# Performance work log

Measured on AMD Instinct MI355X. Metric: run time of the kernel, lower is better.

Reference implementation:

```python
import jax, jax.numpy as jnp
import numpy as np

N_NODES = 50000
N_EDGES = 800000
NUM_LAYERS = 3
NF, EF, QD, H, TD, NT = 256, 64, 128, 64, 32, 64
C = 1.0
EPS = 1e-15


def _expmap0(u, c):
    sc = jnp.sqrt(c)
    n = jnp.maximum(jnp.linalg.norm(u, axis=-1, keepdims=True), EPS)
    return jnp.tanh(sc * n) * u / (sc * n)


def _logmap0(x, c):
    sc = jnp.sqrt(c)
    n = jnp.maximum(jnp.linalg.norm(x, axis=-1, keepdims=True), EPS)
    p = jnp.minimum(sc * n, 1.0 - 1e-5)
    return jnp.arctanh(p) * x / (sc * n)


def setup_inputs() -> dict:
    key = jax.random.key(0)
    ks = jax.random.split(key, 24)
    d = {}
    d['node_features'] = jax.random.normal(ks[0], (N_NODES, NF), jnp.float32)
    d['edge_descriptor'] = jax.random.normal(ks[1], (NT, EF), jnp.float32)
    d['query'] = jax.random.normal(ks[2], (QD,), jnp.float32)
    # params
    d['Wn'] = jax.random.normal(ks[3], (NF, H), jnp.float32) * 0.05  # xavier gain 0.05 in source
    d['bn'] = jnp.zeros((H,), jnp.float32)
    d['tangent_scale'] = jnp.asarray(0.5, jnp.float32)
    d['Wq'] = jax.random.normal(ks[4], (QD, H), jnp.float32) * 0.05
    d['bq'] = jnp.zeros((H,), jnp.float32)
    d['Ws'] = jax.random.normal(ks[5], (EF, TD), jnp.float32) * 0.1
    d['bs'] = jnp.zeros((TD,), jnp.float32)
    d['attn_a'] = jax.random.normal(ks[6], (NUM_LAYERS, 2 * H + TD), jnp.float32) * 0.1
    d['Wmp'] = jax.random.normal(ks[7], (NUM_LAYERS, H, H), jnp.float32) * 0.1
    d['bmp'] = jnp.zeros((NUM_LAYERS, H), jnp.float32)
    d['Wns1'] = jax.random.normal(ks[8], (2 * H, H), jnp.float32) * 0.1
    d['bns1'] = jnp.zeros((H,), jnp.float32)
    d['Wns2'] = jax.random.normal(ks[9], (H, 1), jnp.float32) * 0.1
    d['bns2'] = jnp.zeros((1,), jnp.float32)
    d['Wes1'] = jax.random.normal(ks[10], (2 * H + TD + H, H), jnp.float32) * 0.1
    d['bes1'] = jnp.zeros((H,), jnp.float32)
    d['Wes2'] = jax.random.normal(ks[11], (H, 1), jnp.float32) * 0.1
    d['bes2'] = jnp.zeros((1,), jnp.float32)
    d['edge_index'] = jax.random.randint(ks[12], (2, N_EDGES), 0, N_NODES, jnp.int32)
    d['edge_type'] = jax.random.randint(ks[13], (N_EDGES,), 0, NT, jnp.int32)
    return d


def reference(node_features, edge_descriptor, query, Wn, bn, tangent_scale, Wq, bq,
              Ws, bs, attn_a, Wmp, bmp, Wns1, bns1, Wns2, bns2,
              Wes1, bes1, Wes2, bes2, edge_index, edge_type):
    c = C
    src, dst = edge_index[0], edge_index[1]
    N = node_features.shape[0]
    # node_in + tangent scale + expmap0 onto Poincare ball
    h = _expmap0((node_features @ Wn + bn) * tangent_scale, c)
    q = query @ Wq + bq                       # (H,)
    type_emb = jnp.tanh(edge_descriptor @ Ws + bs)  # (NT, TD) schema encoder
    te = type_emb[edge_type]                  # (E, TD)
    for l in range(NUM_LAYERS):
        ht = _logmap0(h, c)                   # work in tangent space
        feat = jnp.concatenate([ht[src], ht[dst], te], axis=-1)  # (E, 2H+TD)
        s = jax.nn.leaky_relu(feat @ attn_a[l], 0.2)             # (E,)
        m = jax.ops.segment_max(jax.lax.stop_gradient(s), dst, num_segments=N)
        ex = jnp.exp(s - m[dst])
        denom = jax.ops.segment_sum(ex, dst, num_segments=N)
        alpha = ex / (denom[dst] + EPS)       # softmax over incoming edges
        msg = ht @ Wmp[l] + bmp[l]            # (N, H) transform once, gather per-edge
        agg = jax.ops.segment_sum(alpha[:, None] * msg[src], dst, num_segments=N)
        h = _expmap0(jax.nn.relu(agg), c)
    h_flat = _logmap0(h, c)
    q_node = jnp.broadcast_to(q, (N, H))
    node_logits = (jax.nn.relu(jnp.concatenate([h_flat, q_node], -1) @ Wns1 + bns1) @ Wns2 + bns2)[:, 0]
    node_scores = jax.nn.sigmoid(node_logits)
    E = src.shape[0]
    q_edge = jnp.broadcast_to(q, (E, H))
    efeat = jnp.concatenate([h_flat[src], h_flat[dst], te, q_edge], -1)  # (E, 2H+TD+H)
    edge_logits = (jax.nn.relu(efeat @ Wes1 + bes1) @ Wes2 + bes2)[:, 0]
    edge_scores = jax.nn.sigmoid(edge_logits)
    return node_scores, edge_scores, h, type_emb
```

## Files before the change

kernel.cpp:

```cpp
#include <hip/hip_runtime.h>
#include <math.h>

#define NN 50000
#define NE 800000
#define NFD 256
#define HD 64
#define QDD 128
#define TDD 32
#define NTT 64
#define NLAY 3
#define LCLAMP 6.1030340f
#define NBUCK 196
#define SBUCK 6144
#define NPAD (NBUCK * SBUCK)
#define EPB 4096
#define NBINBLK 196
#define PST 72

typedef unsigned int uint;
typedef unsigned short ushort;
typedef __attribute__((ext_vector_type(8))) short bf16x8;
typedef __attribute__((ext_vector_type(4))) float f32x4;

__device__ __forceinline__ ushort f2bf(float f) {
  uint u = __float_as_uint(f);
  uint r = (u + 0x7FFFu + ((u >> 16) & 1u)) >> 16;
  return (ushort)r;
}
__device__ __forceinline__ short f2bfs(float f) { return (short)f2bf(f); }
__device__ __forceinline__ float bf2f(short s) { return __uint_as_float(((uint)(ushort)s) << 16); }
__device__ __forceinline__ float bflo(uint w) { return __uint_as_float(w << 16); }
__device__ __forceinline__ float bfhi(uint w) { return __uint_as_float(w & 0xFFFF0000u); }

__device__ __forceinline__ bf16x8 frag_f32(const float* p) {
  float4 a = *(const float4*)p;
  float4 b = *(const float4*)(p + 4);
  bf16x8 r;
  r[0] = f2bfs(a.x); r[1] = f2bfs(a.y); r[2] = f2bfs(a.z); r[3] = f2bfs(a.w);
  r[4] = f2bfs(b.x); r[5] = f2bfs(b.y); r[6] = f2bfs(b.z); r[7] = f2bfs(b.w);
  return r;
}
__device__ __forceinline__ bf16x8 bfrag_w(const float* W, int k0, int j0, int lane15, int quad) {
  bf16x8 r;
#pragma unroll
  for (int j = 0; j < 8; ++j) r[j] = f2bfs(W[(k0 + quad * 8 + j) * HD + j0 + lane15]);
  return r;
}

__global__ void __launch_bounds__(256) kA(const float* __restrict__ edge_desc, const float* __restrict__ query,
                                          const float* __restrict__ Wq, const float* __restrict__ bq,
                                          const float* __restrict__ Ws, const float* __restrict__ bs,
                                          const float* __restrict__ attn_a,
                                          const float* __restrict__ Wns1, const float* __restrict__ bns1,
                                          const float* __restrict__ Wes1, const float* __restrict__ bes1,
                                          const float* __restrict__ Wmp,
                                          float* __restrict__ out_type_emb,
                                          float* __restrict__ qb, float* __restrict__ ta3,
                                          ushort* __restrict__ Te2bf, ushort* __restrict__ WmpPk) {
  __shared__ float te_l[NTT * TDD];
  __shared__ float q_l[HD];
  __shared__ float qe_l[HD];
  int t = threadIdx.x;
  if (t < HD) {
    float acc = bq[t];
    for (int k = 0; k < QDD; ++k) acc += query[k] * Wq[k * HD + t];
    q_l[t] = acc;
  }
  for (int idx = t; idx < NTT * TDD; idx += 256) {
    int ty = idx / TDD, d = idx % TDD;
    float acc = bs[d];
    for (int k = 0; k < 64; ++k) acc += edge_desc[ty * 64 + k] * Ws[k * TDD + d];
    float v = tanhf(acc);
    te_l[idx] = v;
    out_type_emb[idx] = v;
  }
  __syncthreads();
  if (t < NLAY * NTT) {
    int l = t / NTT, ty = t % NTT;
    float acc = 0.f;
    for (int d = 0; d < TDD; ++d) acc += te_l[ty * TDD + d] * attn_a[l * (2 * HD + TDD) + 2 * HD + d];
    ta3[t] = acc;
  }
  if (t < HD) {
    float a1 = bns1[t], a2 = bes1[t];
    for (int k = 0; k < HD; ++k) {
      a1 += q_l[k] * Wns1[(HD + k) * HD + t];
      a2 += q_l[k] * Wes1[(2 * HD + TDD + k) * HD + t];
    }
    qb[t] = a1;
    qe_l[t] = a2;
  }
  for (int idx = t; idx < NLAY * 4 * 2 * 64 * 8; idx += 256) {
    int j = idx & 7, lane = (idx >> 3) & 63, f = (idx >> 9) & 1, jl = idx >> 10;
    int l = jl >> 2, jt = jl & 3, q = lane >> 4, l15 = lane & 15;
    WmpPk[idx] = f2bf(Wmp[l * HD * HD + (f * 32 + q * 8 + j) * HD + jt * 16 + l15]);
  }
  __syncthreads();
  for (int idx = t; idx < NTT * HD; idx += 256) {
    int ty = idx >> 6, j = idx & 63;
    float acc = qe_l[j];
#pragma unroll
    for (int d = 0; d < TDD; ++d) acc += te_l[ty * TDD + d] * Wes1[(2 * HD + d) * HD + j];
    Te2bf[idx] = f2bf(acc);
  }
}

__device__ void d_bin(int bbid,
                      const int* __restrict__ src,
                      const int* __restrict__ dst,
                      const int* __restrict__ etype,
                      int* __restrict__ bucket_cursor,
                      uint2* __restrict__ ebuf) {
  __shared__ int cntl[NBUCK];
  __shared__ int gbase[NBUCK];
  int t = threadIdx.x;
  for (int i = t; i < NBUCK; i += 256) cntl[i] = 0;
  __syncthreads();
  int e0 = bbid * EPB;
  int dd[16];
  uint pk[16];
  int rk[16];
#pragma unroll
  for (int c = 0; c < 4; ++c) {
    int eb = e0 + c * 1024 + t * 4;
    if (eb < NE) {
      int4 s4 = *(const int4*)&src[eb];
      int4 d4 = *(const int4*)&dst[eb];
      int4 y4 = *(const int4*)&etype[eb];
      int ds[4] = {d4.x, d4.y, d4.z, d4.w};
      int ss[4] = {s4.x, s4.y, s4.z, s4.w};
      int ys[4] = {y4.x, y4.y, y4.z, y4.w};
#pragma unroll
      for (int j = 0; j < 4; ++j) {
        int idx = c * 4 + j;
        int d = ds[j];
        dd[idx] = d;
        pk[idx] = (uint)ss[j] | ((uint)ys[j] << 16) | ((uint)(d & 255) << 22);
        rk[idx] = atomicAdd(&cntl[d >> 8], 1);
      }
    } else {
#pragma unroll
      for (int j = 0; j < 4; ++j) dd[c * 4 + j] = -1;
    }
  }
  __syncthreads();
  if (t < NBUCK && cntl[t] > 0)
    gbase[t] = t * SBUCK + atomicAdd(&bucket_cursor[t], cntl[t]);
  __syncthreads();
#pragma unroll
  for (int i = 0; i < 16; ++i) {
    if (dd[i] >= 0) {
      uint eid = (uint)(e0 + ((i >> 2) << 10) + t * 4 + (i & 3));
      ebuf[gbase[dd[i] >> 8] + rk[i]] = make_uint2(pk[i], eid);
    }
  }
}

__device__ void d_proj(int pbid,
                       const float* __restrict__ X,
                       const float* __restrict__ Wn,
                       const float* __restrict__ bn,
                       const float* __restrict__ ts_p,
                       const ushort* __restrict__ WmpPk,
                       const float* __restrict__ bmp0,
                       const float* __restrict__ attn0,
                       ushort* __restrict__ msgbf,
                       float* __restrict__ p_src,
                       float* __restrict__ p_dst) {
  __shared__ ushort buf[2][64 * PST];
  float* st = (float*)&buf[0][0];
  int t = threadIdx.x;
  int lane = t & 63, wv = t >> 6;
  int lane15 = lane & 15, quad = lane >> 4;
  int n0 = pbid * 64;
  int j0 = wv * 16;
  bf16x8 B[8];
#pragma unroll
  for (int fb = 0; fb < 8; ++fb) B[fb] = bfrag_w(Wn, fb * 32, j0, lane15, quad);

  int srow = t >> 2;
  int scg = (t & 3) * 16;
  int grow = n0 + srow; if (grow >= NN) grow = NN - 1;
  const float* xrow = X + (size_t)grow * NFD + scg;

  f32x4 acc[4];
#pragma unroll
  for (int mt = 0; mt < 4; ++mt) acc[mt] = (f32x4){0.f, 0.f, 0.f, 0.f};

  float4 r0 = *(const float4*)(xrow + 0);
  float4 r1 = *(const float4*)(xrow + 4);
  float4 r2 = *(const float4*)(xrow + 8);
  float4 r3 = *(const float4*)(xrow + 12);

  for (int c = 0; c < 4; ++c) {
    ushort* wp = &buf[c & 1][srow * PST + scg];
    uint4 o0, o1;
    o0.x = (uint)f2bf(r0.x) | ((uint)f2bf(r0.y) << 16);
    o0.y = (uint)f2bf(r0.z) | ((uint)f2bf(r0.w) << 16);
    o0.z = (uint)f2bf(r1.x) | ((uint)f2bf(r1.y) << 16);
    o0.w = (uint)f2bf(r1.z) | ((uint)f2bf(r1.w) << 16);
    o1.x = (uint)f2bf(r2.x) | ((uint)f2bf(r2.y) << 16);
    o1.y = (uint)f2bf(r2.z) | ((uint)f2bf(r2.w) << 16);
    o1.z = (uint)f2bf(r3.x) | ((uint)f2bf(r3.y) << 16);
    o1.w = (uint)f2bf(r3.z) | ((uint)f2bf(r3.w) << 16);
    *(uint4*)wp = o0;
    *(uint4*)(wp + 8) = o1;
    if (c < 3) {
      const float* nx = xrow + (c + 1) * 64;
      r0 = *(const float4*)(nx + 0);
      r1 = *(const float4*)(nx + 4);
      r2 = *(const float4*)(nx + 8);
      r3 = *(const float4*)(nx + 12);
    }
    __syncthreads();
    const ushort* bp = &buf[c & 1][0];
#pragma unroll
    for (int mt = 0; mt < 4; ++mt) {
#pragma unroll
      for (int ks = 0; ks < 2; ++ks) {
        bf16x8 A = *(const bf16x8*)&bp[(mt * 16 + lane15) * PST + ks * 32 + quad * 8];
        acc[mt] = __builtin_amdgcn_mfma_f32_16x16x32_bf16(A, B[c * 2 + ks], acc[mt], 0, 0, 0);
      }
    }
  }
  __syncthreads();
  float ts = ts_p[0];
  float vb = bn[j0 + lane15];
#pragma unroll
  for (int mt = 0; mt < 4; ++mt)
#pragma unroll
    for (int i = 0; i < 4; ++i)
      st[(mt * 16 + quad * 4 + i) * PST + j0 + lane15] = (acc[mt][i] + vb) * ts;
  __syncthreads();
  {
    int r = t >> 2, p = t & 3;
    float* rp = &st[r * PST + p * 16];
    float4 v0 = *(const float4*)(rp + 0);
    float4 v1 = *(const float4*)(rp + 4);
    float4 v2 = *(const float4*)(rp + 8);
    float4 v3 = *(const float4*)(rp + 12);
    float ssq = v0.x*v0.x + v0.y*v0.y + v0.z*v0.z + v0.w*v0.w
              + v1.x*v1.x + v1.y*v1.y + v1.z*v1.z + v1.w*v1.w
              + v2.x*v2.x + v2.y*v2.y + v2.z*v2.z + v2.w*v2.w
              + v3.x*v3.x + v3.y*v3.y + v3.z*v3.z + v3.w*v3.w;
    ssq += __shfl_xor(ssq, 1, 64);
    ssq += __shfl_xor(ssq, 2, 64);
    float nu = fmaxf(sqrtf(ssq), 1e-15f);
    float sc = fminf(nu, LCLAMP) / nu;
    *(float4*)(rp + 0) = make_float4(v0.x*sc, v0.y*sc, v0.z*sc, v0.w*sc);
    *(float4*)(rp + 4) = make_float4(v1.x*sc, v1.y*sc, v1.z*sc, v1.w*sc);
    *(float4*)(rp + 8) = make_float4(v2.x*sc, v2.y*sc, v2.z*sc, v2.w*sc);
    *(float4*)(rp + 12) = make_float4(v3.x*sc, v3.y*sc, v3.z*sc, v3.w*sc);
  }
  __syncthreads();
  {
    bf16x8 Bm0[4], Bm1[4];
    float vbm[4];
#pragma unroll
    for (int jt = 0; jt < 4; ++jt) {
      Bm0[jt] = *(const bf16x8*)&WmpPk[((jt * 2 + 0) * 64 + lane) * 8];
      Bm1[jt] = *(const bf16x8*)&WmpPk[((jt * 2 + 1) * 64 + lane) * 8];
      vbm[jt] = bmp0[jt * 16 + lane15];
    }
    int mrow = wv * 16 + lane15;
    bf16x8 A0 = frag_f32(&st[mrow * PST + quad * 8]);
    bf16x8 A1 = frag_f32(&st[mrow * PST + 32 + quad * 8]);
#pragma unroll
    for (int jt = 0; jt < 4; ++jt) {
      f32x4 z = {0.f, 0.f, 0.f, 0.f};
      z = __builtin_amdgcn_mfma_f32_16x16x32_bf16(A0, Bm0[jt], z, 0, 0, 0);
      z = __builtin_amdgcn_mfma_f32_16x16x32_bf16(A1, Bm1[jt], z, 0, 0, 0);
#pragma unroll
      for (int i = 0; i < 4; ++i) {
        int r = n0 + wv * 16 + quad * 4 + i;
        if (r < NN) msgbf[(size_t)r * HD + jt * 16 + lane15] = f2bf(z[i] + vbm[jt]);
      }
    }
    float4 a1l = *(const float4*)&attn0[quad * 8];
    float4 a1h = *(const float4*)&attn0[quad * 8 + 4];
    float4 a1l2 = *(const float4*)&attn0[32 + quad * 8];
    float4 a1h2 = *(const float4*)&attn0[32 + quad * 8 + 4];
    float4 a2l = *(const float4*)&attn0[64 + quad * 8];
    float4 a2h = *(const float4*)&attn0[64 + quad * 8 + 4];
    float4 a2l2 = *(const float4*)&attn0[96 + quad * 8];
    float4 a2h2 = *(const float4*)&attn0[96 + quad * 8 + 4];
    float p1 = bf2f(A0[0])*a1l.x + bf2f(A0[1])*a1l.y + bf2f(A0[2])*a1l.z + bf2f(A0[3])*a1l.w
             + bf2f(A0[4])*a1h.x + bf2f(A0[5])*a1h.y + bf2f(A0[6])*a1h.z + bf2f(A0[7])*a1h.w
             + bf2f(A1[0])*a1l2.x + bf2f(A1[1])*a1l2.y + bf2f(A1[2])*a1l2.z + bf2f(A1[3])*a1l2.w
             + bf2f(A1[4])*a1h2.x + bf2f(A1[5])*a1h2.y + bf2f(A1[6])*a1h2.z + bf2f(A1[7])*a1h2.w;
    float p2 = bf2f(A0[0])*a2l.x + bf2f(A0[1])*a2l.y + bf2f(A0[2])*a2l.z + bf2f(A0[3])*a2l.w
             + bf2f(A0[4])*a2h.x + bf2f(A0[5])*a2h.y + bf2f(A0[6])*a2h.z + bf2f(A0[7])*a2h.w
             + bf2f(A1[0])*a2l2.x + bf2f(A1[1])*a2l2.y + bf2f(A1[2])*a2l2.z + bf2f(A1[3])*a2l2.w
             + bf2f(A1[4])*a2h2.x + bf2f(A1[5])*a2h2.y + bf2f(A1[6])*a2h2.z + bf2f(A1[7])*a2h2.w;
    p1 += __shfl_xor(p1, 16, 64); p1 += __shfl_xor(p1, 32, 64);
    p2 += __shfl_xor(p2, 16, 64); p2 += __shfl_xor(p2, 32, 64);
    int prow = n0 + mrow;
    if (quad == 0 && prow < NN) { p_src[prow] = p1; p_dst[prow] = p2; }
  }
}

__global__ void __launch_bounds__(256) kE(const int* __restrict__ src, const int* __restrict__ dst,
                                          const int* __restrict__ etype, int* __restrict__ bucket_cursor,
                                          uint2* __restrict__ ebuf,
                                          const float* __restrict__ X, const float* __restrict__ Wn,
                                          const float* __restrict__ bn, const float* __restrict__ ts_p,
                                          const ushort* __restrict__ WmpPk, const float* __restrict__ bmp0,
                                          const float* __restrict__ attn0,
                                          ushort* __restrict__ msgbf,
                                          float* __restrict__ p_src, float* __restrict__ p_dst) {
  if (blockIdx.x < NBINBLK)
    d_bin(blockIdx.x, src, dst, etype, bucket_cursor, ebuf);
  else
    d_proj(blockIdx.x - NBINBLK, X, Wn, bn, ts_p, WmpPk, bmp0, attn0, msgbf, p_src, p_dst);
}

__global__ void __launch_bounds__(256) k_scatter2(const int* __restrict__ bucket_cursor,
                                                  const uint2* __restrict__ ebuf,
                                                  uint* __restrict__ csr,
                                                  uint* __restrict__ csr_eid,
                                                  uint2* __restrict__ rdeg) {
  __shared__ int cnt_l[256];
  __shared__ int curs[256];
  __shared__ int wsum[4], woff[4];
  int b = blockIdx.x;
  int t = threadIdx.x;
  int base = b * SBUCK;
  int cb = bucket_cursor[b];
  cnt_l[t] = 0;
  __syncthreads();
  for (int i = t; i < cb; i += 256)
    atomicAdd(&cnt_l[(ebuf[base + i].x >> 22) & 255], 1);
  __syncthreads();
  int v = cnt_l[t];
  int lane = t & 63, wid = t >> 6;
  int x = v;
#pragma unroll
  for (int off = 1; off < 64; off <<= 1) {
    int y = __shfl_up(x, off, 64);
    if (lane >= off) x += y;
  }
  if (lane == 63) wsum[wid] = x;
  __syncthreads();
  if (t == 0) {
    int a = 0;
    for (int i = 0; i < 4; ++i) { woff[i] = a; a += wsum[i]; }
  }
  __syncthreads();
  int loff = woff[wid] + (x - v);
  int n = (b << 8) + t;
  if (n < NN) rdeg[n] = make_uint2((uint)(base + loff), (uint)v);
  curs[t] = base + loff;
  __syncthreads();
  for (int i = t; i < cb; i += 256) {
    uint2 e = ebuf[base + i];
    int j = (e.x >> 22) & 255;
    int pos = atomicAdd(&curs[j], 1);
    csr[pos] = e.x & 0x3FFFFFu;
    csr_eid[pos] = e.y;
  }
}

template <int FUSE>
__global__ void __launch_bounds__(256) k_agg(const uint2* __restrict__ rdeg,
                                             const uint* __restrict__ csr,
                                             const float* __restrict__ p_src,
                                             const float* __restrict__ p_dst,
                                             const float* __restrict__ ta_l,
                                             const ushort* __restrict__ msgbf,
                                             float* __restrict__ s_buf,
                                             const ushort* __restrict__ WmpPk_next,
                                             const float* __restrict__ bmp_next,
                                             const float* __restrict__ attn_next,
                                             ushort* __restrict__ msg_out,
                                             float* __restrict__ p_src_out,
                                             float* __restrict__ p_dst_out,
                                             float* __restrict__ ht_out) {
  __shared__ float v_lds[16][68];
  __shared__ float exs[4][64];
  __shared__ uint  sis[4][64];
  int t = threadIdx.x;
  int lane = t & 63, wv = t >> 6;
  int nloc = t >> 5;
  int half = (lane >> 5) & 1;
  int l32 = lane & 31;
  int lq = lane & 7;
  int lg32 = (lane >> 3) & 3;
  int n = blockIdx.x * 8 + nloc;
  uint2 rd = rdeg[n];
  int start = (int)rd.x;
  int deg = (int)rd.y;
  int end = start + deg;
  float pd = p_dst[n];
  float acc[8];
#pragma unroll
  for (int u = 0; u < 8; ++u) acc[u] = 0.f;
  float exsum = 0.f;

  if (deg <= 32) {
    bool valid = l32 < deg;
    float s = -3.4e38f;
    int sidx = 0;
    if (valid) {
      uint pk = csr[start + l32];
      sidx = (int)(pk & 0xFFFFu);
      int ty = (int)(pk >> 16);
      float v = p_src[sidx] + pd + ta_l[ty];
      s = (v > 0.f) ? v : 0.2f * v;
    }
    float m = s;
#pragma unroll
    for (int off = 16; off >= 1; off >>= 1) m = fmaxf(m, __shfl_xor(m, off, 64));
    float ex = valid ? __expf(s - m) : 0.f;
    exsum = ex;
    if (valid) { exs[wv][lane] = ex; sis[wv][lane] = (uint)sidx; }
    for (int it = 0; it < deg; it += 4) {
      int el = it + lg32;
      if (el < deg) {
        float exk = exs[wv][half * 32 + el];
        int sk = (int)sis[wv][half * 32 + el];
        uint4 mv = *(const uint4*)&msgbf[(size_t)sk * HD + lq * 8];
        acc[0] += exk * bflo(mv.x); acc[1] += exk * bfhi(mv.x);
        acc[2] += exk * bflo(mv.y); acc[3] += exk * bfhi(mv.y);
        acc[4] += exk * bflo(mv.z); acc[5] += exk * bfhi(mv.z);
        acc[6] += exk * bflo(mv.w); acc[7] += exk * bfhi(mv.w);
      }
    }
  } else {
    float m = -3.4e38f;
    for (int base = start; base < end; base += 32) {
      int i = base + l32;
      float s = -3.4e38f;
      if (i < end) {
        uint pk = csr[i];
        int sidx = (int)(pk & 0xFFFFu);
        int ty = (int)(pk >> 16);
        float v = p_src[sidx] + pd + ta_l[ty];
        s = (v > 0.f) ? v : 0.2f * v;
        s_buf[i] = s;
      }
      m = fmaxf(m, s);
    }
#pragma unroll
    for (int off = 16; off >= 1; off >>= 1) m = fmaxf(m, __shfl_xor(m, off, 64));
    for (int base = start; base < end; base += 32) {
      int i = base + l32;
      if (i < end) {
        float ex = __expf(s_buf[i] - m);
        s_buf[i] = ex;
        exsum += ex;
      }
    }
    for (int it = start; it < end; it += 4) {
      int el = it + lg32;
      if (el < end) {
        float exk = s_buf[el];
        int sk = (int)(csr[el] & 0xFFFFu);
        uint4 mv = *(const uint4*)&msgbf[(size_t)sk * HD + lq * 8];
        acc[0] += exk * bflo(mv.x); acc[1] += exk * bfhi(mv.x);
        acc[2] += exk * bflo(mv.y); acc[3] += exk * bfhi(mv.y);
        acc[4] += exk * bflo(mv.z); acc[5] += exk * bfhi(mv.z);
        acc[6] += exk * bflo(mv.w); acc[7] += exk * bfhi(mv.w);
      }
    }
  }
#pragma unroll
  for (int u = 0; u < 8; ++u) {
    acc[u] += __shfl_xor(acc[u], 8, 64);
    acc[u] += __shfl_xor(acc[u], 16, 64);
  }
#pragma unroll
  for (int off = 16; off >= 1; off >>= 1) exsum += __shfl_xor(exsum, off, 64);
  float inv = 1.f / (exsum + 1e-15f);
  float ss = 0.f;
#pragma unroll
  for (int u = 0; u < 8; ++u) {
    float v = fmaxf(acc[u] * inv, 0.f);
    acc[u] = v;
    ss += v * v;
  }
  ss += __shfl_xor(ss, 1, 64);
  ss += __shfl_xor(ss, 2, 64);
  ss += __shfl_xor(ss, 4, 64);
  float nu = fmaxf(sqrtf(ss), 1e-15f);
  float sc = fminf(nu, LCLAMP) / nu;

  if constexpr (FUSE == 0) {
    if (l32 < 8) {
      *(float4*)&ht_out[(size_t)n * HD + l32 * 8] =
          make_float4(acc[0] * sc, acc[1] * sc, acc[2] * sc, acc[3] * sc);
      *(float4*)&ht_out[(size_t)n * HD + l32 * 8 + 4] =
          make_float4(acc[4] * sc, acc[5] * sc, acc[6] * sc, acc[7] * sc);
    }
  } else {
    float hb[8];
#pragma unroll
    for (int u = 0; u < 8; ++u) hb[u] = bf2f((short)f2bf(acc[u] * sc));
    float4 a1a = *(const float4*)&attn_next[lq * 8];
    float4 a1b = *(const float4*)&attn_next[lq * 8 + 4];
    float4 a2a = *(const float4*)&attn_next[64 + lq * 8];
    float4 a2b = *(const float4*)&attn_next[64 + lq * 8 + 4];
    float p1 = hb[0]*a1a.x + hb[1]*a1a.y + hb[2]*a1a.z + hb[3]*a1a.w
             + hb[4]*a1b.x + hb[5]*a1b.y + hb[6]*a1b.z + hb[7]*a1b.w;
    float p2 = hb[0]*a2a.x + hb[1]*a2a.y + hb[2]*a2a.z + hb[3]*a2a.w
             + hb[4]*a2b.x + hb[5]*a2b.y + hb[6]*a2b.z + hb[7]*a2b.w;
    p1 += __shfl_xor(p1, 1, 64); p1 += __shfl_xor(p1, 2, 64); p1 += __shfl_xor(p1, 4, 64);
    p2 += __shfl_xor(p2, 1, 64); p2 += __shfl_xor(p2, 2, 64); p2 += __shfl_xor(p2, 4, 64);
    if (l32 == 0) { p_src_out[n] = p1; p_dst_out[n] = p2; }
    if (l32 < 8) {
      *(float4*)&v_lds[nloc][l32 * 8] =
          make_float4(acc[0] * sc, acc[1] * sc, acc[2] * sc, acc[3] * sc);
      *(float4*)&v_lds[nloc][l32 * 8 + 4] =
          make_float4(acc[4] * sc, acc[5] * sc, acc[6] * sc, acc[7] * sc);
    }
    __syncthreads();
    int lane15 = lane & 15, quad = lane >> 4;
    bf16x8 A0 = frag_f32(&v_lds[lane15][quad * 8]);
    bf16x8 A1 = frag_f32(&v_lds[lane15][32 + quad * 8]);
    bf16x8 B0 = *(const bf16x8*)&WmpPk_next[(wv * 2 + 0) * 512 + lane * 8];
    bf16x8 B1 = *(const bf16x8*)&WmpPk_next[(wv * 2 + 1) * 512 + lane * 8];
    f32x4 z = {0.f, 0.f, 0.f, 0.f};
    z = __builtin_amdgcn_mfma_f32_16x16x32_bf16(A0, B0, z, 0, 0, 0);
    z = __builtin_amdgcn_mfma_f32_16x16x32_bf16(A1, B1, z, 0, 0, 0);
    float vbm = bmp_next[wv * 16 + lane15];
    if (quad < 2) {
      int nb = blockIdx.x * 8;
#pragma unroll
      for (int i = 0; i < 4; ++i)
        msg_out[(size_t)(nb + quad * 4 + i) * HD + wv * 16 + lane15] = f2bf(z[i] + vbm);
    }
  }
}

__global__ void __launch_bounds__(256) k_score(const float* __restrict__ ht,
                                               const float* __restrict__ Wns1,
                                               const float* __restrict__ qb,
                                               const float* __restrict__ Wns2,
                                               const float* __restrict__ bns2,
                                               const float* __restrict__ Wes1,
                                               float* __restrict__ node_scores,
                                               float* __restrict__ h_out,
                                               ushort* __restrict__ Asrc,
                                               ushort* __restrict__ Adst) {
  int t = threadIdx.x;
  int lane = t & 63, wv = t >> 6;
  int lane15 = lane & 15, quad = lane >> 4;
  int n0 = blockIdx.x * 64;
  int m0 = n0 + wv * 16;
  int row = m0 + lane15;
  int rowc = row < NN ? row : NN - 1;
  bf16x8 A0 = frag_f32(ht + (size_t)rowc * HD + quad * 8);
  bf16x8 A1 = frag_f32(ht + (size_t)rowc * HD + 32 + quad * 8);

  {
    f32x4 acc[4];
#pragma unroll
    for (int jt = 0; jt < 4; ++jt) {
      bf16x8 b0 = bfrag_w(Wns1, 0, jt * 16, lane15, quad);
      bf16x8 b1 = bfrag_w(Wns1, 32, jt * 16, lane15, quad);
      f32x4 z = {0.f, 0.f, 0.f, 0.f};
      z = __builtin_amdgcn_mfma_f32_16x16x32_bf16(A0, b0, z, 0, 0, 0);
      z = __builtin_amdgcn_mfma_f32_16x16x32_bf16(A1, b1, z, 0, 0, 0);
      acc[jt] = z;
    }
    float vqb[4], vw2[4];
#pragma unroll
    for (int jt = 0; jt < 4; ++jt) { vqb[jt] = qb[jt * 16 + lane15]; vw2[jt] = Wns2[jt * 16 + lane15]; }
    float b2 = bns2[0];
#pragma unroll
    for (int i = 0; i < 4; ++i) {
      float si = 0.f;
#pragma unroll
      for (int jt = 0; jt < 4; ++jt) si += fmaxf(acc[jt][i] + vqb[jt], 0.f) * vw2[jt];
      si += __shfl_xor(si, 1, 64);
      si += __shfl_xor(si, 2, 64);
      si += __shfl_xor(si, 4, 64);
      si += __shfl_xor(si, 8, 64);
      int r = m0 + quad * 4 + i;
      if (lane15 == 0 && r < NN) node_scores[r] = 1.f / (1.f + __expf(-(si + b2)));
    }
  }
  {
#pragma unroll
    for (int jt = 0; jt < 4; ++jt) {
      bf16x8 b0 = bfrag_w(Wes1, 0, jt * 16, lane15, quad);
      bf16x8 b1 = bfrag_w(Wes1, 32, jt * 16, lane15, quad);
      f32x4 z = {0.f, 0.f, 0.f, 0.f};
      z = __builtin_amdgcn_mfma_f32_16x16x32_bf16(A0, b0, z, 0, 0, 0);
      z = __builtin_amdgcn_mfma_f32_16x16x32_bf16(A1, b1, z, 0, 0, 0);
#pragma unroll
      for (int i = 0; i < 4; ++i) {
        int r = m0 + quad * 4 + i;
        if (r < NN) Asrc[(size_t)r * HD + jt * 16 + lane15] = f2bf(z[i]);
      }
    }
  }
  {
    const float* W = Wes1 + 64 * HD;
#pragma unroll
    for (int jt = 0; jt < 4; ++jt) {
      bf16x8 b0 = bfrag_w(W, 0, jt * 16, lane15, quad);
      bf16x8 b1 = bfrag_w(W, 32, jt * 16, lane15, quad);
      f32x4 z = {0.f, 0.f, 0.f, 0.f};
      z = __builtin_amdgcn_mfma_f32_16x16x32_bf16(A0, b0, z, 0, 0, 0);
      z = __builtin_amdgcn_mfma_f32_16x16x32_bf16(A1, b1, z, 0, 0, 0);
#pragma unroll
      for (int i = 0; i < 4; ++i) {
        int r = m0 + quad * 4 + i;
        if (r < NN) Adst[(size_t)r * HD + jt * 16 + lane15] = f2bf(z[i]);
      }
    }
  }
  {
    int r = t >> 2, p = t & 3;
    int gr = n0 + r;
    int grc = gr < NN ? gr : NN - 1;
    const float* rp = ht + (size_t)grc * HD + p * 16;
    float4 v0 = *(const float4*)(rp + 0);
    float4 v1 = *(const float4*)(rp + 4);
    float4 v2 = *(const float4*)(rp + 8);
    float4 v3 = *(const float4*)(rp + 12);
    float ssq = v0.x*v0.x + v0.y*v0.y + v0.z*v0.z + v0.w*v0.w
              + v1.x*v1.x + v1.y*v1.y + v1.z*v1.z + v1.w*v1.w
              + v2.x*v2.x + v2.y*v2.y + v2.z*v2.z + v2.w*v2.w
              + v3.x*v3.x + v3.y*v3.y + v3.z*v3.z + v3.w*v3.w;
    ssq += __shfl_xor(ssq, 1, 64);
    ssq += __shfl_xor(ssq, 2, 64);
    float nu = fmaxf(sqrtf(ssq), 1e-15f);
    float hs = tanhf(nu) / nu;
    if (gr < NN) {
      float* op = h_out + (size_t)gr * HD + p * 16;
      *(float4*)(op + 0)  = make_float4(v0.x*hs, v0.y*hs, v0.z*hs, v0.w*hs);
      *(float4*)(op + 4)  = make_float4(v1.x*hs, v1.y*hs, v1.z*hs, v1.w*hs);
      *(float4*)(op + 8)  = make_float4(v2.x*hs, v2.y*hs, v2.z*hs, v2.w*hs);
      *(float4*)(op + 12) = make_float4(v3.x*hs, v3.y*hs, v3.z*hs, v3.w*hs);
    }
  }
}

__global__ void __launch_bounds__(256) k_edge(const uint2* __restrict__ rdeg,
                                              const uint* __restrict__ csr,
                                              const uint* __restrict__ csr_eid,
                                              const ushort* __restrict__ Asrc,
                                              const ushort* __restrict__ Adst,
                                              const ushort* __restrict__ Te2bf,
                                              const float* __restrict__ Wes2,
                                              const float* __restrict__ bes2,
                                              float* __restrict__ edge_scores) {
  int t = threadIdx.x;
  int lane = t & 63;
  int n = (blockIdx.x * 256 + t) >> 6;
  if (n >= NN) return;
  int lq = lane & 7, lg = lane >> 3;
  uint2 rd = rdeg[n];
  int start = (int)rd.x;
  int deg = (int)rd.y;
  if (deg == 0) return;
  int end = start + deg;
  uint4 bv = *(const uint4*)&Adst[(size_t)n * HD + lq * 8];
  const float* wp = &Wes2[lq * 8];
  float4 w0 = *(const float4*)wp;
  float4 w1 = *(const float4*)(wp + 4);
  float b2 = bes2[0];
  for (int it = start; it < end; it += 8) {
    int e = it + lg;
    bool valid = e < end;
    float p = 0.f;
    if (valid) {
      uint pk = csr[e];
      int si = (int)(pk & 0xFFFFu);
      int ty = (int)((pk >> 16) & 0x3Fu);
      uint4 av = *(const uint4*)&Asrc[(size_t)si * HD + lq * 8];
      uint4 tv = *(const uint4*)&Te2bf[ty * HD + lq * 8];
      p += fmaxf(bflo(av.x) + bflo(bv.x) + bflo(tv.x), 0.f) * w0.x;
      p += fmaxf(bfhi(av.x) + bfhi(bv.x) + bfhi(tv.x), 0.f) * w0.y;
      p += fmaxf(bflo(av.y) + bflo(bv.y) + bflo(tv.y), 0.f) * w0.z;
      p += fmaxf(bfhi(av.y) + bfhi(bv.y) + bfhi(tv.y), 0.f) * w0.w;
      p += fmaxf(bflo(av.z) + bflo(bv.z) + bflo(tv.z), 0.f) * w1.x;
      p += fmaxf(bfhi(av.z) + bfhi(bv.z) + bfhi(tv.z), 0.f) * w1.y;
      p += fmaxf(bflo(av.w) + bflo(bv.w) + bflo(tv.w), 0.f) * w1.z;
      p += fmaxf(bfhi(av.w) + bfhi(bv.w) + bfhi(tv.w), 0.f) * w1.w;
    }
    p += __shfl_xor(p, 1, 64);
    p += __shfl_xor(p, 2, 64);
    p += __shfl_xor(p, 4, 64);
    if (valid && lq == 0) edge_scores[csr_eid[e]] = 1.f / (1.f + __expf(-(p + b2)));
  }
}

extern "C" void kernel_launch(void* const* d_in, const int* in_sizes, int n_in,
                              void* d_out, int out_size, void* d_ws, size_t ws_size,
                              hipStream_t stream) {
  const float* node_features = (const float*)d_in[0];
  const float* edge_desc = (const float*)d_in[1];
  const float* query = (const float*)d_in[2];
  const float* Wn = (const float*)d_in[3];
  const float* bn = (const float*)d_in[4];
  const float* ts = (const float*)d_in[5];
  const float* Wq = (const float*)d_in[6];
  const float* bq = (const float*)d_in[7];
  const float* Ws_ = (const float*)d_in[8];
  const float* bs = (const float*)d_in[9];
  const float* attn_a = (const float*)d_in[10];
  const float* Wmp = (const float*)d_in[11];
  const float* bmp = (const float*)d_in[12];
  const float* Wns1 = (const float*)d_in[13];
  const float* bns1 = (const float*)d_in[14];
  const float* Wns2 = (const float*)d_in[15];
  const float* bns2 = (const float*)d_in[16];
  const float* Wes1 = (const float*)d_in[17];
  const float* bes1 = (const float*)d_in[18];
  const float* Wes2 = (const float*)d_in[19];
  const float* bes2 = (const float*)d_in[20];
  const int* edge_index = (const int*)d_in[21];
  const int* etype = (const int*)d_in[22];
  const int* src = edge_index;
  const int* dst = edge_index + NE;

  float* out_ns = (float*)d_out;
  float* out_es = out_ns + NN;
  float* out_h = out_es + NE;
  float* out_te = out_h + (size_t)NN * HD;

  char* w = (char*)d_ws;
  auto alloc = [&](size_t bytes) {
    char* p = w;
    w += (bytes + 1023) & ~(size_t)1023;
    return p;
  };
  float* ht_f = (float*)alloc((size_t)NN * HD * 4);
  ushort* msg0 = (ushort*)alloc((size_t)NN * HD * 2);
  ushort* msg1 = (ushort*)alloc((size_t)NN * HD * 2);
  ushort* Asrc = (ushort*)alloc((size_t)NN * HD * 2);
  ushort* Adst = (ushort*)alloc((size_t)NN * HD * 2);
  float* pA = (float*)alloc(NN * 4);
  float* pdA = (float*)alloc(NN * 4);
  float* pB = (float*)alloc(NN * 4);
  float* pdB = (float*)alloc(NN * 4);
  float* s_buf = (float*)alloc((size_t)NPAD * 4);
  float* qb = (float*)alloc(HD * 4);
  float* ta3 = (float*)alloc(NLAY * NTT * 4);
  ushort* Te2bf = (ushort*)alloc(NTT * HD * 2);
  ushort* WmpPk = (ushort*)alloc(NLAY * 4096 * 2);
  int* bucket_cursor = (int*)alloc(NBUCK * 4);
  uint2* rdeg = (uint2*)alloc((size_t)NN * 8);
  uint* csr = (uint*)alloc((size_t)NPAD * 4);
  uint* csr_eid = (uint*)alloc((size_t)NPAD * 4);
  uint2* ebuf = (uint2*)Asrc;

  hipMemsetAsync(bucket_cursor, 0, NBUCK * 4, stream);
  kA<<<1, 256, 0, stream>>>(edge_desc, query, Wq, bq, Ws_, bs, attn_a,
                            Wns1, bns1, Wes1, bes1, Wmp, out_te, qb, ta3, Te2bf, WmpPk);
  kE<<<NBINBLK + (NN + 63) / 64, 256, 0, stream>>>(src, dst, etype, bucket_cursor, ebuf,
                                                   node_features, Wn, bn, ts, WmpPk,
                                                   bmp, attn_a, msg0, pA, pdA);
  k_scatter2<<<NBUCK, 256, 0, stream>>>(bucket_cursor, ebuf, csr, csr_eid, rdeg);

  const int AGG_GRID = NN / 8;
  k_agg<1><<<AGG_GRID, 256, 0, stream>>>(rdeg, csr, pA, pdA, ta3 + 0 * NTT, msg0, s_buf,
                                         WmpPk + 1 * 4096, bmp + 1 * HD,
                                         attn_a + 1 * (2 * HD + TDD),
                                         msg1, pB, pdB, nullptr);
  k_agg<1><<<AGG_GRID, 256, 0, stream>>>(rdeg, csr, pB, pdB, ta3 + 1 * NTT, msg1, s_buf,
                                         WmpPk + 2 * 4096, bmp + 2 * HD,
                                         attn_a + 2 * (2 * HD + TDD),
                                         msg0, pA, pdA, nullptr);
  k_agg<0><<<AGG_GRID, 256, 0, stream>>>(rdeg, csr, pA, pdA, ta3 + 2 * NTT, msg0, s_buf,
                                         nullptr, nullptr, nullptr,
                                         nullptr, nullptr, nullptr, ht_f);

  k_score<<<(NN + 63) / 64, 256, 0, stream>>>(ht_f, Wns1, qb, Wns2, bns2, Wes1,
                                              out_ns, out_h, Asrc, Adst);
  k_edge<<<(NN + 3) / 4, 256, 0, stream>>>(rdeg, csr, csr_eid, Asrc, Adst, Te2bf,
                                           Wes2, bes2, out_es);
}
```

Baseline: 322.3 us.

## Fold setup kernel into binning kernel and fuse scoring into last aggregation

The single-block setup kernel kA becomes an extra block of the combined binning/projection kernel, and d_proj now packs the layer-0 Wmp weights itself instead of reading them pre-packed. The separate k_score kernel is removed: the final aggregation layer keeps the tangent vectors in LDS and directly computes the expmap output, node scores and the Asrc/Adst edge-MLP projections with MFMA, using weights pre-packed to bf16 in setup. This drops two launches and the fp32 ht round trip through global memory. In exchange it adds a block barrier and extra work to the aggregation kernel, and the MFMA tiles use only half their rows because each block holds 8 nodes.

```diff
diff --git a/kernel.cpp b/kernel.cpp
--- a/kernel.cpp
+++ b/kernel.cpp
@@ -15,6 +15,7 @@
 #define NPAD (NBUCK * SBUCK)
 #define EPB 4096
 #define NBINBLK 196
+#define NPROJ 782
 #define PST 72
 
 typedef unsigned int uint;
@@ -47,16 +48,18 @@
   return r;
 }
 
-__global__ void __launch_bounds__(256) kA(const float* __restrict__ edge_desc, const float* __restrict__ query,
-                                          const float* __restrict__ Wq, const float* __restrict__ bq,
-                                          const float* __restrict__ Ws, const float* __restrict__ bs,
-                                          const float* __restrict__ attn_a,
-                                          const float* __restrict__ Wns1, const float* __restrict__ bns1,
-                                          const float* __restrict__ Wes1, const float* __restrict__ bes1,
-                                          const float* __restrict__ Wmp,
-                                          float* __restrict__ out_type_emb,
-                                          float* __restrict__ qb, float* __restrict__ ta3,
-                                          ushort* __restrict__ Te2bf, ushort* __restrict__ WmpPk) {
+__device__ void d_setup(const float* __restrict__ edge_desc, const float* __restrict__ query,
+                        const float* __restrict__ Wq, const float* __restrict__ bq,
+                        const float* __restrict__ Ws, const float* __restrict__ bs,
+                        const float* __restrict__ attn_a,
+                        const float* __restrict__ Wns1, const float* __restrict__ bns1,
+                        const float* __restrict__ Wes1, const float* __restrict__ bes1,
+                        const float* __restrict__ Wmp,
+                        float* __restrict__ out_type_emb,
+                        float* __restrict__ qb, float* __restrict__ ta3,
+                        ushort* __restrict__ Te2bf, ushort* __restrict__ WmpPk,
+                        ushort* __restrict__ WnsPk, ushort* __restrict__ WesaPk,
+                        ushort* __restrict__ WesbPk) {
   __shared__ float te_l[NTT * TDD];
   __shared__ float q_l[HD];
   __shared__ float qe_l[HD];
@@ -94,6 +97,14 @@
     int j = idx & 7, lane = (idx >> 3) & 63, f = (idx >> 9) & 1, jl = idx >> 10;
     int l = jl >> 2, jt = jl & 3, q = lane >> 4, l15 = lane & 15;
     WmpPk[idx] = f2bf(Wmp[l * HD * HD + (f * 32 + q * 8 + j) * HD + jt * 16 + l15]);
+  }
+  for (int idx = t; idx < 4 * 2 * 64 * 8; idx += 256) {
+    int j = idx & 7, lane = (idx >> 3) & 63, f = (idx >> 9) & 1, jt = (idx >> 10) & 3;
+    int q = lane >> 4, l15 = lane & 15;
+    int row = f * 32 + q * 8 + j, col = jt * 16 + l15;
+    WnsPk[idx]  = f2bf(Wns1[row * HD + col]);
+    WesaPk[idx] = f2bf(Wes1[row * HD + col]);
+    WesbPk[idx] = f2bf(Wes1[(64 + row) * HD + col]);
   }
   __syncthreads();
   for (int idx = t; idx < NTT * HD; idx += 256) {
@@ -161,7 +172,7 @@
                        const float* __restrict__ Wn,
                        const float* __restrict__ bn,
                        const float* __restrict__ ts_p,
-                       const ushort* __restrict__ WmpPk,
+                       const float* __restrict__ Wmp0,
                        const float* __restrict__ bmp0,
                        const float* __restrict__ attn0,
                        ushort* __restrict__ msgbf,
@@ -258,8 +269,8 @@
     float vbm[4];
 #pragma unroll
     for (int jt = 0; jt < 4; ++jt) {
-      Bm0[jt] = *(const bf16x8*)&WmpPk[((jt * 2 + 0) * 64 + lane) * 8];
-      Bm1[jt] = *(const bf16x8*)&WmpPk[((jt * 2 + 1) * 64 + lane) * 8];
+      Bm0[jt] = bfrag_w(Wmp0, 0, jt * 16, lane15, quad);
+      Bm1[jt] = bfrag_w(Wmp0, 32, jt * 16, lane15, quad);
       vbm[jt] = bmp0[jt * 16 + lane15];
     }
     int mrow = wv * 16 + lane15;
@@ -304,14 +315,27 @@
                                           uint2* __restrict__ ebuf,
                                           const float* __restrict__ X, const float* __restrict__ Wn,
                                           const float* __restrict__ bn, const float* __restrict__ ts_p,
-                                          const ushort* __restrict__ WmpPk, const float* __restrict__ bmp0,
-                                          const float* __restrict__ attn0,
+                                          const float* __restrict__ Wmp, const float* __restrict__ bmp,
+                                          const float* __restrict__ attn_a,
                                           ushort* __restrict__ msgbf,
-                                          float* __restrict__ p_src, float* __restrict__ p_dst) {
+                                          float* __restrict__ p_src, float* __restrict__ p_dst,
+                                          const float* __restrict__ edge_desc, const float* __restrict__ query,
+                                          const float* __restrict__ Wq, const float* __restrict__ bq,
+                                          const float* __restrict__ Ws, const float* __restrict__ bs,
+                                          const float* __restrict__ Wns1, const float* __restrict__ bns1,
+                                          const float* __restrict__ Wes1, const float* __restrict__ bes1,
+                                          float* __restrict__ out_type_emb,
+                                          float* __restrict__ qb, float* __restrict__ ta3,
+                                          ushort* __restrict__ Te2bf, ushort* __restrict__ WmpPk,
+                                          ushort* __restrict__ WnsPk, ushort* __restrict__ WesaPk,
+                                          ushort* __restrict__ WesbPk) {
   if (blockIdx.x < NBINBLK)
     d_bin(blockIdx.x, src, dst, etype, bucket_cursor, ebuf);
+  else if (blockIdx.x < NBINBLK + NPROJ)
+    d_proj(blockIdx.x - NBINBLK, X, Wn, bn, ts_p, Wmp, bmp, attn_a, msgbf, p_src, p_dst);
   else
-    d_proj(blockIdx.x - NBINBLK, X, Wn, bn, ts_p, WmpPk, bmp0, attn0, msgbf, p_src, p_dst);
+    d_setup(edge_desc, query, Wq, bq, Ws, bs, attn_a, Wns1, bns1, Wes1, bes1, Wmp,
+            out_type_emb, qb, ta3, Te2bf, WmpPk, WnsPk, WesaPk, WesbPk);
 }
 
 __global__ void __launch_bounds__(256) k_scatter2(const int* __restrict__ bucket_cursor,
@@ -374,10 +398,20 @@
                                              ushort* __restrict__ msg_out,
                                              float* __restrict__ p_src_out,
                                              float* __restrict__ p_dst_out,
-                                             float* __restrict__ ht_out) {
+                                             const float* __restrict__ qb,
+                                             const float* __restrict__ Wns2,
+                                             const float* __restrict__ bns2,
+                                             const ushort* __restrict__ WnsPk,
+                                             const ushort* __restrict__ WesaPk,
+                                             const ushort* __restrict__ WesbPk,
+                                             float* __restrict__ node_scores,
+                                             float* __restrict__ h_out,
+                                             ushort* __restrict__ Asrc,
+                                             ushort* __restrict__ Adst) {
   __shared__ float v_lds[16][68];
   __shared__ float exs[4][64];
   __shared__ uint  sis[4][64];
+  __shared__ float sc_part[8][4];
   int t = threadIdx.x;
   int lane = t & 63, wv = t >> 6;
   int nloc = t >> 5;
@@ -486,10 +520,85 @@
 
   if constexpr (FUSE == 0) {
     if (l32 < 8) {
-      *(float4*)&ht_out[(size_t)n * HD + l32 * 8] =
+      *(float4*)&v_lds[nloc][l32 * 8] =
           make_float4(acc[0] * sc, acc[1] * sc, acc[2] * sc, acc[3] * sc);
-      *(float4*)&ht_out[(size_t)n * HD + l32 * 8 + 4] =
+      *(float4*)&v_lds[nloc][l32 * 8 + 4] =
           make_float4(acc[4] * sc, acc[5] * sc, acc[6] * sc, acc[7] * sc);
+    }
+    __syncthreads();
+    int lane15 = lane & 15, quad = lane >> 4;
+    int nb = blockIdx.x * 8;
+    if (t < 32) {
+      int r = t >> 2, p = t & 3;
+      const float* rp = &v_lds[r][p * 16];
+      float4 v0 = *(const float4*)(rp + 0);
+      float4 v1 = *(const float4*)(rp + 4);
+      float4 v2 = *(const float4*)(rp + 8);
+      float4 v3 = *(const float4*)(rp + 12);
+      float ssq = v0.x*v0.x + v0.y*v0.y + v0.z*v0.z + v0.w*v0.w
+                + v1.x*v1.x + v1.y*v1.y + v1.z*v1.z + v1.w*v1.w
+                + v2.x*v2.x + v2.y*v2.y + v2.z*v2.z + v2.w*v2.w
+                + v3.x*v3.x + v3.y*v3.y + v3.z*v3.z + v3.w*v3.w;
+      ssq += __shfl_xor(ssq, 1, 64);
+      ssq += __shfl_xor(ssq, 2, 64);
+      float nu2 = fmaxf(sqrtf(ssq), 1e-15f);
+      float hs = tanhf(nu2) / nu2;
+      float* op = h_out + (size_t)(nb + r) * HD + p * 16;
+      *(float4*)(op + 0)  = make_float4(v0.x*hs, v0.y*hs, v0.z*hs, v0.w*hs);
+      *(float4*)(op + 4)  = make_float4(v1.x*hs, v1.y*hs, v1.z*hs, v1.w*hs);
+      *(float4*)(op + 8)  = make_float4(v2.x*hs, v2.y*hs, v2.z*hs, v2.w*hs);
+      *(float4*)(op + 12) = make_float4(v3.x*hs, v3.y*hs, v3.z*hs, v3.w*hs);
+    }
+    bf16x8 A0 = frag_f32(&v_lds[lane15][quad * 8]);
+    bf16x8 A1 = frag_f32(&v_lds[lane15][32 + quad * 8]);
+    {
+      bf16x8 B0 = *(const bf16x8*)&WnsPk[(wv * 2 + 0) * 512 + lane * 8];
+      bf16x8 B1 = *(const bf16x8*)&WnsPk[(wv * 2 + 1) * 512 + lane * 8];
+      f32x4 z = {0.f, 0.f, 0.f, 0.f};
+      z = __builtin_amdgcn_mfma_f32_16x16x32_bf16(A0, B0, z, 0, 0, 0);
+      z = __builtin_amdgcn_mfma_f32_16x16x32_bf16(A1, B1, z, 0, 0, 0);
+      float vqb = qb[wv * 16 + lane15];
+      float vw2 = Wns2[wv * 16 + lane15];
+      if (quad < 2) {
+#pragma unroll
+        for (int i = 0; i < 4; ++i) {
+          float part = fmaxf(z[i] + vqb, 0.f) * vw2;
+          part += __shfl_xor(part, 1, 64);
+          part += __shfl_xor(part, 2, 64);
+          part += __shfl_xor(part, 4, 64);
+          part += __shfl_xor(part, 8, 64);
+          if (lane15 == 0) sc_part[quad * 4 + i][wv] = part;
+        }
+      }
+    }
+    {
+      bf16x8 B0 = *(const bf16x8*)&WesaPk[(wv * 2 + 0) * 512 + lane * 8];
+      bf16x8 B1 = *(const bf16x8*)&WesaPk[(wv * 2 + 1) * 512 + lane * 8];
+      f32x4 z = {0.f, 0.f, 0.f, 0.f};
+      z = __builtin_amdgcn_mfma_f32_16x16x32_bf16(A0, B0, z, 0, 0, 0);
+      z = __builtin_amdgcn_mfma_f32_16x16x32_bf16(A1, B1, z, 0, 0, 0);
+      if (quad < 2) {
+#pragma unroll
+        for (int i = 0; i < 4; ++i)
+          Asrc[(size_t)(nb + quad * 4 + i) * HD + wv * 16 + lane15] = f2bf(z[i]);
+      }
+    }
+    {
+      bf16x8 B0 = *(const bf16x8*)&WesbPk[(wv * 2 + 0) * 512 + lane * 8];
+      bf16x8 B1 = *(const bf16x8*)&WesbPk[(wv * 2 + 1) * 512 + lane * 8];
+      f32x4 z = {0.f, 0.f, 0.f, 0.f};
+      z = __builtin_amdgcn_mfma_f32_16x16x32_bf16(A0, B0, z, 0, 0, 0);
+      z = __builtin_amdgcn_mfma_f32_16x16x32_bf16(A1, B1, z, 0, 0, 0);
+      if (quad < 2) {
+#pragma unroll
+        for (int i = 0; i < 4; ++i)
+          Adst[(size_t)(nb + quad * 4 + i) * HD + wv * 16 + lane15] = f2bf(z[i]);
+      }
+    }
+    __syncthreads();
+    if (t < 8) {
+      float si = sc_part[t][0] + sc_part[t][1] + sc_part[t][2] + sc_part[t][3];
+      node_scores[nb + t] = 1.f / (1.f + __expf(-(si + bns2[0])));
     }
   } else {
     float hb[8];
@@ -527,112 +636,6 @@
 #pragma unroll
       for (int i = 0; i < 4; ++i)
         msg_out[(size_t)(nb + quad * 4 + i) * HD + wv * 16 + lane15] = f2bf(z[i] + vbm);
-    }
-  }
-}
-
-__global__ void __launch_bounds__(256) k_score(const float* __restrict__ ht,
-                                               const float* __restrict__ Wns1,
-                                               const float* __restrict__ qb,
-                                               const float* __restrict__ Wns2,
-                                               const float* __restrict__ bns2,
-                                               const float* __restrict__ Wes1,
-                                               float* __restrict__ node_scores,
-                                               float* __restrict__ h_out,
-                                               ushort* __restrict__ Asrc,
-                                               ushort* __restrict__ Adst) {
-  int t = threadIdx.x;
-  int lane = t & 63, wv = t >> 6;
-  int lane15 = lane & 15, quad = lane >> 4;
-  int n0 = blockIdx.x * 64;
-  int m0 = n0 + wv * 16;
-  int row = m0 + lane15;
-  int rowc = row < NN ? row : NN - 1;
-  bf16x8 A0 = frag_f32(ht + (size_t)rowc * HD + quad * 8);
-  bf16x8 A1 = frag_f32(ht + (size_t)rowc * HD + 32 + quad * 8);
-
-  {
-    f32x4 acc[4];
-#pragma unroll
-    for (int jt = 0; jt < 4; ++jt) {
-      bf16x8 b0 = bfrag_w(Wns1, 0, jt * 16, lane15, quad);
-      bf16x8 b1 = bfrag_w(Wns1, 32, jt * 16, lane15, quad);
-      f32x4 z = {0.f, 0.f, 0.f, 0.f};
-      z = __builtin_amdgcn_mfma_f32_16x16x32_bf16(A0, b0, z, 0, 0, 0);
-      z = __builtin_amdgcn_mfma_f32_16x16x32_bf16(A1, b1, z, 0, 0, 0);
-      acc[jt] = z;
-    }
-    float vqb[4], vw2[4];
-#pragma unroll
-    for (int jt = 0; jt < 4; ++jt) { vqb[jt] = qb[jt * 16 + lane15]; vw2[jt] = Wns2[jt * 16 + lane15]; }
-    float b2 = bns2[0];
-#pragma unroll
-    for (int i = 0; i < 4; ++i) {
-      float si = 0.f;
-#pragma unroll
-      for (int jt = 0; jt < 4; ++jt) si += fmaxf(acc[jt][i] + vqb[jt], 0.f) * vw2[jt];
-      si += __shfl_xor(si, 1, 64);
-      si += __shfl_xor(si, 2, 64);
-      si += __shfl_xor(si, 4, 64);
-      si += __shfl_xor(si, 8, 64);
-      int r = m0 + quad * 4 + i;
-      if (lane15 == 0 && r < NN) node_scores[r] = 1.f / (1.f + __expf(-(si + b2)));
-    }
-  }
-  {
-#pragma unroll
-    for (int jt = 0; jt < 4; ++jt) {
-      bf16x8 b0 = bfrag_w(Wes1, 0, jt * 16, lane15, quad);
-      bf16x8 b1 = bfrag_w(Wes1, 32, jt * 16, lane15, quad);
-      f32x4 z = {0.f, 0.f, 0.f, 0.f};
-      z = __builtin_amdgcn_mfma_f32_16x16x32_bf16(A0, b0, z, 0, 0, 0);
-      z = __builtin_amdgcn_mfma_f32_16x16x32_bf16(A1, b1, z, 0, 0, 0);
-#pragma unroll
-      for (int i = 0; i < 4; ++i) {
-        int r = m0 + quad * 4 + i;
-        if (r < NN) Asrc[(size_t)r * HD + jt * 16 + lane15] = f2bf(z[i]);
-      }
-    }
-  }
-  {
-    const float* W = Wes1 + 64 * HD;
-#pragma unroll
-    for (int jt = 0; jt < 4; ++jt) {
-      bf16x8 b0 = bfrag_w(W, 0, jt * 16, lane15, quad);
-      bf16x8 b1 = bfrag_w(W, 32, jt * 16, lane15, quad);
-      f32x4 z = {0.f, 0.f, 0.f, 0.f};
-      z = __builtin_amdgcn_mfma_f32_16x16x32_bf16(A0, b0, z, 0, 0, 0);
-      z = __builtin_amdgcn_mfma_f32_16x16x32_bf16(A1, b1, z, 0, 0, 0);
-#pragma unroll
-      for (int i = 0; i < 4; ++i) {
-        int r = m0 + quad * 4 + i;
-        if (r < NN) Adst[(size_t)r * HD + jt * 16 + lane15] = f2bf(z[i]);
-      }
-    }
-  }
-  {
-    int r = t >> 2, p = t & 3;
-    int gr = n0 + r;
-    int grc = gr < NN ? gr : NN - 1;
-    const float* rp = ht + (size_t)grc * HD + p * 16;
-    float4 v0 = *(const float4*)(rp + 0);
-    float4 v1 = *(const float4*)(rp + 4);
-    float4 v2 = *(const float4*)(rp + 8);
-    float4 v3 = *(const float4*)(rp + 12);
-    float ssq = v0.x*v0.x + v0.y*v0.y + v0.z*v0.z + v0.w*v0.w
-              + v1.x*v1.x + v1.y*v1.y + v1.z*v1.z + v1.w*v1.w
-              + v2.x*v2.x + v2.y*v2.y + v2.z*v2.z + v2.w*v2.w
-              + v3.x*v3.x + v3.y*v3.y + v3.z*v3.z + v3.w*v3.w;
-    ssq += __shfl_xor(ssq, 1, 64);
-    ssq += __shfl_xor(ssq, 2, 64);
-    float nu = fmaxf(sqrtf(ssq), 1e-15f);
-    float hs = tanhf(nu) / nu;
-    if (gr < NN) {
-      float* op = h_out + (size_t)gr * HD + p * 16;
-      *(float4*)(op + 0)  = make_float4(v0.x*hs, v0.y*hs, v0.z*hs, v0.w*hs);
-      *(float4*)(op + 4)  = make_float4(v1.x*hs, v1.y*hs, v1.z*hs, v1.w*hs);
-      *(float4*)(op + 8)  = make_float4(v2.x*hs, v2.y*hs, v2.z*hs, v2.w*hs);
-      *(float4*)(op + 12) = make_float4(v3.x*hs, v3.y*hs, v3.z*hs, v3.w*hs);
     }
   }
 }
@@ -727,7 +730,6 @@
     w += (bytes + 1023) & ~(size_t)1023;
     return p;
   };
-  float* ht_f = (float*)alloc((size_t)NN * HD * 4);
   ushort* msg0 = (ushort*)alloc((size_t)NN * HD * 2);
   ushort* msg1 = (ushort*)alloc((size_t)NN * HD * 2);
   ushort* Asrc = (ushort*)alloc((size_t)NN * HD * 2);
@@ -741,6 +743,9 @@
   float* ta3 = (float*)alloc(NLAY * NTT * 4);
   ushort* Te2bf = (ushort*)alloc(NTT * HD * 2);
   ushort* WmpPk = (ushort*)alloc(NLAY * 4096 * 2);
+  ushort* WnsPk = (ushort*)alloc(4096 * 2);
+  ushort* WesaPk = (ushort*)alloc(4096 * 2);
+  ushort* WesbPk = (ushort*)alloc(4096 * 2);
   int* bucket_cursor = (int*)alloc(NBUCK * 4);
   uint2* rdeg = (uint2*)alloc((size_t)NN * 8);
   uint* csr = (uint*)alloc((size_t)NPAD * 4);
@@ -748,28 +753,34 @@
   uint2* ebuf = (uint2*)Asrc;
 
   hipMemsetAsync(bucket_cursor, 0, NBUCK * 4, stream);
-  kA<<<1, 256, 0, stream>>>(edge_desc, query, Wq, bq, Ws_, bs, attn_a,
-                            Wns1, bns1, Wes1, bes1, Wmp, out_te, qb, ta3, Te2bf, WmpPk);
-  kE<<<NBINBLK + (NN + 63) / 64, 256, 0, stream>>>(src, dst, etype, bucket_cursor, ebuf,
-                                                   node_features, Wn, bn, ts, WmpPk,
-                                                   bmp, attn_a, msg0, pA, pdA);
+  kE<<<NBINBLK + NPROJ + 1, 256, 0, stream>>>(src, dst, etype, bucket_cursor, ebuf,
+                                              node_features, Wn, bn, ts, Wmp, bmp, attn_a,
+                                              msg0, pA, pdA,
+                                              edge_desc, query, Wq, bq, Ws_, bs,
+                                              Wns1, bns1, Wes1, bes1,
+                                              out_te, qb, ta3, Te2bf, WmpPk,
+                                              WnsPk, WesaPk, WesbPk);
   k_scatter2<<<NBUCK, 256, 0, stream>>>(bucket_cursor, ebuf, csr, csr_eid, rdeg);
 
   const int AGG_GRID = NN / 8;
   k_agg<1><<<AGG_GRID, 256, 0, stream>>>(rdeg, csr, pA, pdA, ta3 + 0 * NTT, msg0, s_buf,
                                          WmpPk + 1 * 4096, bmp + 1 * HD,
                                          attn_a + 1 * (2 * HD + TDD),
-                                         msg1, pB, pdB, nullptr);
+                                         msg1, pB, pdB,
+                                         nullptr, nullptr, nullptr, nullptr, nullptr,
+                                         nullptr, nullptr, nullptr, nullptr, nullptr);
   k_agg<1><<<AGG_GRID, 256, 0, stream>>>(rdeg, csr, pB, pdB, ta3 + 1 * NTT, msg1, s_buf,
                                          WmpPk + 2 * 4096, bmp + 2 * HD,
                                          attn_a + 2 * (2 * HD + TDD),
-                                         msg0, pA, pdA, nullptr);
+                                         msg0, pA, pdA,
+                                         nullptr, nullptr, nullptr, nullptr, nullptr,
+                                         nullptr, nullptr, nullptr, nullptr, nullptr);
   k_agg<0><<<AGG_GRID, 256, 0, stream>>>(rdeg, csr, pA, pdA, ta3 + 2 * NTT, msg0, s_buf,
                                          nullptr, nullptr, nullptr,
-                                         nullptr, nullptr, nullptr, ht_f);
-
-  k_score<<<(NN + 63) / 64, 256, 0, stream>>>(ht_f, Wns1, qb, Wns2, bns2, Wes1,
-                                              out_ns, out_h, Asrc, Adst);
+                                         nullptr, nullptr, nullptr,
+                                         qb, Wns2, bns2, WnsPk, WesaPk, WesbPk,
+                                         out_ns, out_h, Asrc, Adst);
+
   k_edge<<<(NN + 3) / 4, 256, 0, stream>>>(rdeg, csr, csr_eid, Asrc, Adst, Te2bf,
                                            Wes2, bes2, out_es);
 }
```

Result: faster. 313.7 us (-2.6%).
